# Kernel tuning notes

Measured on AMD Instinct MI355X. Metric: run time of the kernel, lower is better.

Reference implementation:

```python
import jax, jax.numpy as jnp
import numpy as np

WORD_VOCAB = 100000
TAG_VOCAB = 50
WD = 300
TD = 100
EMB = WD + TD          # 400: LSTM input size AND hidden size
H = EMB
L = 512


def setup_inputs() -> dict:
    key = jax.random.key(0)
    ks = jax.random.split(key, 16)
    def p(k, shape):
        return jax.random.normal(k, shape, dtype=jnp.float32) * 0.05
    return {
        "words_idx_tensor": jax.random.randint(ks[0], (1, L), 0, WORD_VOCAB),
        "tags_idx_tensor": jax.random.randint(ks[1], (1, L), 0, TAG_VOCAB),
        "max_length": L,
        "word_emb": p(ks[2], (WORD_VOCAB, WD)),
        "tag_emb": p(ks[3], (TAG_VOCAB, TD)),
        # stacked [fwd, bwd] directions per layer (PyTorch LSTM gate order i,f,g,o)
        "w_ih_l0": p(ks[4], (2, 4 * H, EMB)),
        "w_hh_l0": p(ks[5], (2, 4 * H, H)),
        "b_ih_l0": p(ks[6], (2, 4 * H)),
        "b_hh_l0": p(ks[7], (2, 4 * H)),
        "w_ih_l1": p(ks[8], (2, 4 * H, 2 * H)),
        "w_hh_l1": p(ks[9], (2, 4 * H, H)),
        "b_ih_l1": p(ks[10], (2, 4 * H)),
        "b_hh_l1": p(ks[11], (2, 4 * H)),
        "fc1_w": p(ks[12], (1, 4 * H)),
        "fc1_b": p(ks[13], (1,)),
    }


def _lstm_dir(x, w_ih, w_hh, b_ih, b_hh, reverse):
    # x: [T, in]. Precompute input projections once (hoisted out of scan).
    xi = x @ w_ih.T + b_ih + b_hh  # [T, 4H]
    Hn = w_hh.shape[1]

    def step(carry, g_in):
        h, c = carry
        g = g_in + h @ w_hh.T
        i, f, gg, o = jnp.split(g, 4, axis=-1)
        c = jax.nn.sigmoid(f) * c + jax.nn.sigmoid(i) * jnp.tanh(gg)
        h = jax.nn.sigmoid(o) * jnp.tanh(c)
        return (h, c), h

    init = (jnp.zeros((Hn,), x.dtype), jnp.zeros((Hn,), x.dtype))
    _, hs = jax.lax.scan(step, init, xi, reverse=reverse)
    return hs  # [T, H]


def _bilstm(x, w_ih, w_hh, b_ih, b_hh):
    fwd = _lstm_dir(x, w_ih[0], w_hh[0], b_ih[0], b_hh[0], False)
    bwd = _lstm_dir(x, w_ih[1], w_hh[1], b_ih[1], b_hh[1], True)
    return jnp.concatenate([fwd, bwd], axis=-1)  # [T, 2H]


def reference(words_idx_tensor, tags_idx_tensor, max_length, word_emb, tag_emb,
              w_ih_l0, w_hh_l0, b_ih_l0, b_hh_l0,
              w_ih_l1, w_hh_l1, b_ih_l1, b_hh_l1,
              fc1_w, fc1_b):
    # Embedding lookup + concat; batch dim of size 1 squeezed (torch's
    # view(shape[1], shape[0], -1) yields [L, 1, emb] for the LSTM).
    x = jnp.concatenate([word_emb[words_idx_tensor[0]],
                         tag_emb[tags_idx_tensor[0]]], axis=-1)  # [L, EMB]

    h = _bilstm(x, w_ih_l0, w_hh_l0, b_ih_l0, b_hh_l0)   # [L, 2H]
    h = _bilstm(h, w_ih_l1, w_hh_l1, b_ih_l1, b_hh_l1)   # [L, 2H]

    # Pairwise edge scores: tanh(W @ [h_i; h_j] + b).
    # Split W into head/dep halves -> two small GEMMs + broadcast outer-sum,
    # avoiding the O(L^2 * 4H) concatenated feature tensor.
    two_h = fc1_w.shape[1] // 2
    s = h @ fc1_w[:, :two_h].T   # [L, 1]
    t = h @ fc1_w[:, two_h:].T   # [L, 1]
    scores = jnp.tanh(s[:, None, :] + t[None, :, :] + fc1_b)  # [L, L, 1]
    # torch stacks (i outer, j inner) -> [L*L, 1, 1]
    return scores.reshape(max_length * max_length, 1, 1)
```

## Files before the change

kernel.cpp:

```cpp
#include <hip/hip_runtime.h>

#define SEQ 512
#define HID 400
#define GATES 1600
#define E1 800
#define TEAM 25
#define RECGRID 256
#define ROWS 64
#define HSL 16

__device__ __forceinline__ float bf2f(unsigned short u) {
    return __uint_as_float(((unsigned)u) << 16);
}
__device__ __forceinline__ unsigned short f2bf(float f) {
    unsigned u = __float_as_uint(f);
    u += 0x7FFFu + ((u >> 16) & 1u);
    return (unsigned short)(u >> 16);
}
__device__ __forceinline__ float sigm(float x) { return 1.f / (1.f + __expf(-x)); }
__device__ __forceinline__ float tanh_f(float x) {
    float xc = fminf(fmaxf(x, -15.f), 15.f);
    float e = __expf(2.f * xc);
    return (e - 1.f) / (e + 1.f);
}
__device__ __forceinline__ float loadx(const void* p, size_t i, int isbf) {
    return isbf ? bf2f(((const unsigned short*)p)[i]) : ((const float*)p)[i];
}

__global__ void detect_kernel(const unsigned short* __restrict__ wemb,
                              unsigned* __restrict__ dtf,
                              unsigned* __restrict__ syncz ) {
    __shared__ int cnt;
    if (threadIdx.x < 32) syncz[threadIdx.x] = 0u;
    if (threadIdx.x == 0) cnt = 0;
    __syncthreads();
    int pass = 0;
    for (int i = 0; i < 8; ++i) {
        unsigned short u = wemb[threadIdx.x * 8 + i];
        int e = (u >> 7) & 0xFF;
        pass += (e >= 100 && e <= 130) ? 1 : 0;
    }
    atomicAdd(&cnt, pass);
    __syncthreads();
    if (threadIdx.x == 0) *dtf = (cnt >= 1843) ? 1u : 0u;
}

__global__ void embed_kernel(const int* __restrict__ words, const int* __restrict__ tags,
                             const void* __restrict__ wemb, const void* __restrict__ temb,
                             float* __restrict__ x ,
                             const unsigned* __restrict__ dtf) {
    int t = blockIdx.x;
    int w = words[t], g = tags[t];
    int isbf = (int)*dtf;
    for (int k = threadIdx.x; k < HID; k += blockDim.x) {
        float v = (k < 300) ? loadx(wemb, (size_t)w * 300 + k, isbf)
                            : loadx(temb, (size_t)g * 100 + (k - 300), isbf);
        x[(size_t)t * HID + k] = v;
    }
}

__global__ __launch_bounds__(256) void proj_kernel(
        const void* __restrict__ Araw, int tagged,
        const void* __restrict__ Wraw ,
        const void* __restrict__ bihRaw, const void* __restrict__ bhhRaw,
        float* __restrict__ xi ,
        int K, const unsigned* __restrict__ dtf) {
    const int isbf = (int)*dtf;
    __shared__ float As[16][132];
    __shared__ float Ws[16][68];
    int tid = threadIdx.x;
    int t0 = blockIdx.x * 128, n0 = blockIdx.y * 64, dir = blockIdx.z;
    int arow = tid >> 1, akoff = (tid & 1) * 8;
    int wrow = tid >> 2, wkoff = (tid & 3) * 4;
    int tx = (tid & 15) * 4;
    int ty = (tid >> 4) * 8;

    const float* Af = (const float*)Araw + (size_t)(t0 + arow) * K + akoff;
    const unsigned long long* At = (const unsigned long long*)Araw +
                                   (size_t)(t0 + arow) * K + akoff;
    size_t wbase = (size_t)(dir * GATES + n0 + wrow) * K + wkoff;
    const float* Wf = (const float*)Wraw + wbase;
    const unsigned short* Wh = (const unsigned short*)Wraw + wbase;

    float acc[8][4] = {};
    for (int k0 = 0; k0 < K; k0 += 16) {
        float av8[8];
        if (tagged) {
            ulonglong2 q0 = *(const ulonglong2*)(At + k0);
            ulonglong2 q1 = *(const ulonglong2*)(At + k0 + 2);
            ulonglong2 q2 = *(const ulonglong2*)(At + k0 + 4);
            ulonglong2 q3 = *(const ulonglong2*)(At + k0 + 6);
            av8[0] = __uint_as_float((unsigned)q0.x); av8[1] = __uint_as_float((unsigned)q0.y);
            av8[2] = __uint_as_float((unsigned)q1.x); av8[3] = __uint_as_float((unsigned)q1.y);
            av8[4] = __uint_as_float((unsigned)q2.x); av8[5] = __uint_as_float((unsigned)q2.y);
            av8[6] = __uint_as_float((unsigned)q3.x); av8[7] = __uint_as_float((unsigned)q3.y);
        } else {
            float4 a0 = *(const float4*)(Af + k0);
            float4 a1 = *(const float4*)(Af + k0 + 4);
            av8[0] = a0.x; av8[1] = a0.y; av8[2] = a0.z; av8[3] = a0.w;
            av8[4] = a1.x; av8[5] = a1.y; av8[6] = a1.z; av8[7] = a1.w;
        }
        float4 wv;
        if (isbf) {
            ushort4 w4 = *(const ushort4*)(Wh + k0);
            wv = make_float4(bf2f(w4.x), bf2f(w4.y), bf2f(w4.z), bf2f(w4.w));
        } else {
            wv = *(const float4*)(Wf + k0);
        }
        __syncthreads();
#pragma unroll
        for (int i = 0; i < 8; ++i) As[akoff + i][arow] = av8[i];
        Ws[wkoff + 0][wrow] = wv.x; Ws[wkoff + 1][wrow] = wv.y;
        Ws[wkoff + 2][wrow] = wv.z; Ws[wkoff + 3][wrow] = wv.w;
        __syncthreads();
#pragma unroll
        for (int kk = 0; kk < 16; ++kk) {
            float4 alo = *(const float4*)&As[kk][ty];
            float4 ahi = *(const float4*)&As[kk][ty + 4];
            float4 w4  = *(const float4*)&Ws[kk][tx];
            float av[8] = {alo.x, alo.y, alo.z, alo.w, ahi.x, ahi.y, ahi.z, ahi.w};
            float wvv[4] = {w4.x, w4.y, w4.z, w4.w};
#pragma unroll
            for (int i = 0; i < 8; ++i)
#pragma unroll
                for (int j = 0; j < 4; ++j)
                    acc[i][j] = fmaf(av[i], wvv[j], acc[i][j]);
        }
    }
    float bias[4];
#pragma unroll
    for (int j = 0; j < 4; ++j) {
        int n = n0 + tx + j;
        bias[j] = loadx(bihRaw, dir * GATES + n, isbf) + loadx(bhhRaw, dir * GATES + n, isbf);
    }
    float* xout = xi + (size_t)dir * SEQ * GATES;
#pragma unroll
    for (int i = 0; i < 8; ++i) {
        int t = t0 + ty + i;
        float4 o = make_float4(acc[i][0] + bias[0], acc[i][1] + bias[1],
                               acc[i][2] + bias[2], acc[i][3] + bias[3]);
        *(float4*)&xout[(size_t)t * GATES + n0 + tx] = o;
    }
}

struct SyncArea { unsigned cnt[8]; unsigned claim[2]; unsigned pad[6]; };

__global__ __launch_bounds__(512, 2) void rec_kernel(
        const float* __restrict__ xi ,
        const void* __restrict__ whhRaw ,
        unsigned long long* __restrict__ hx  ,
        unsigned long long* __restrict__ hx2 ,
        unsigned tagbase, SyncArea* __restrict__ sy,
        const unsigned* __restrict__ dtf) {
    int tid = threadIdx.x;
    __shared__ int role[2];
    if (tid == 0) {
        unsigned xcd = __builtin_amdgcn_s_getreg((3 << 11) | 20) & 0xFu;
        unsigned rank = atomicAdd(&sy->cnt[xcd], 1u);
        unsigned group = rank / TEAM;
        unsigned key = 1u + xcd * 64u + group;
        if ((rank % TEAM) == TEAM - 1) {
            unsigned prev = atomicCAS(&sy->claim[0], 0u, key);
            if (prev != 0u) atomicCAS(&sy->claim[1], 0u, key);
        }
        int dir = -1;
        while (dir < 0) {
            unsigned c0 = __hip_atomic_load(&sy->claim[0], __ATOMIC_RELAXED,
                                            __HIP_MEMORY_SCOPE_AGENT);
            unsigned c1 = __hip_atomic_load(&sy->claim[1], __ATOMIC_RELAXED,
                                            __HIP_MEMORY_SCOPE_AGENT);
            if (c0 == key) dir = 0;
            else if (c1 == key) dir = 1;
            else if (c0 != 0u && c1 != 0u) dir = 2;
        }
        role[0] = dir;
        role[1] = (int)(rank % TEAM);
    }
    __syncthreads();
    const int dir = role[0];
    const int wg  = role[1];
    if (dir == 2) return;

    const int chunk = tid & 15;
    const int rg    = tid >> 4;
    const int isbf  = (int)*dtf;
    const int dirHID = dir * HID;

    __shared__ __align__(16) float hbuf[16 * 28];
    __shared__ __align__(16) float partials[ROWS][20];
    __shared__ __align__(16) float gates[ROWS];

    float wv[2][25];
#pragma unroll
    for (int r = 0; r < 2; ++r) {
        int lr = rg * 2 + r;
        int jj = lr >> 2, gg = lr & 3;
        int grow = gg * HID + wg * HSL + jj;
        size_t base = ((size_t)dir * GATES + grow) * HID + chunk * 25;
        if (isbf) {
            const unsigned short* p = (const unsigned short*)whhRaw + base;
#pragma unroll
            for (int c = 0; c < 25; ++c) wv[r][c] = bf2f(p[c]);
        } else {
            const float* p = (const float*)whhRaw + base;
#pragma unroll
            for (int c = 0; c < 25; ++c) wv[r][c] = p[c];
        }
    }

    int xrow = 0;
    if (tid < ROWS) { int jj = tid >> 2, gg = tid & 3; xrow = gg * HID + wg * HSL + jj; }
    const int hIdx = (tid / 25) * 28 + (tid % 25);
    const float* xibase = xi + (size_t)dir * SEQ * GATES;
    const int pl = tid - 448;
    float cstate = 0.f;
    size_t myelem = dirHID + wg * HSL + (pl & 15);

#pragma unroll 1
    for (int k = 0; k < SEQ; ++k) {
        int t = dir ? (SEQ - 1 - k) : k;
        float xiv = 0.f;
        if (tid < ROWS) xiv = xibase[(size_t)t * GATES + xrow];

        if (k > 0) {
            int tprev = dir ? (t + 1) : (t - 1);
            if (tid < HID) {
                const unsigned want = tagbase + (unsigned)k;
                size_t eidx = (size_t)tprev * E1 + dirHID + tid;
                const volatile unsigned long long* p =
                    (const volatile unsigned long long*)&hx[eidx];
                unsigned long long w;
                int spin = 0;
                for (;;) {
                    w = *p;
                    if ((unsigned)(w >> 32) == want) break;
                    if (++spin >= 24) {
                        w = __hip_atomic_load(&hx2[eidx], __ATOMIC_RELAXED,
                                              __HIP_MEMORY_SCOPE_AGENT);
                        if ((unsigned)(w >> 32) == want) break;
                        spin = 0;
                    }
                }
                hbuf[hIdx] = __uint_as_float((unsigned)w);
            }
        } else {
            if (tid < HID) hbuf[hIdx] = 0.f;
        }
        __syncthreads();

        const float* hb = &hbuf[chunk * 28];
        float4 h4a = *(const float4*)(hb + 0);
        float4 h4b = *(const float4*)(hb + 4);
        float4 h4c = *(const float4*)(hb + 8);
        float4 h4d = *(const float4*)(hb + 12);
        float4 h4e = *(const float4*)(hb + 16);
        float4 h4f = *(const float4*)(hb + 20);
        float hv[25] = {h4a.x, h4a.y, h4a.z, h4a.w, h4b.x, h4b.y, h4b.z, h4b.w,
                        h4c.x, h4c.y, h4c.z, h4c.w, h4d.x, h4d.y, h4d.z, h4d.w,
                        h4e.x, h4e.y, h4e.z, h4e.w, h4f.x, h4f.y, h4f.z, h4f.w,
                        hb[24]};
        float acc0 = 0.f, acc1 = 0.f;
#pragma unroll
        for (int c = 0; c < 25; ++c) {
            acc0 = fmaf(wv[0][c], hv[c], acc0);
            acc1 = fmaf(wv[1][c], hv[c], acc1);
        }
        partials[rg * 2 + 0][chunk] = acc0;
        partials[rg * 2 + 1][chunk] = acc1;
        __syncthreads();

        if (tid < ROWS) {
            const float4* pr = (const float4*)&partials[tid][0];
            float4 p0 = pr[0], p1 = pr[1], p2 = pr[2], p3 = pr[3];
            float s = p0.x + p0.y + p0.z + p0.w
                    + p1.x + p1.y + p1.z + p1.w
                    + p2.x + p2.y + p2.z + p2.w
                    + p3.x + p3.y + p3.z + p3.w;
            gates[tid] = s + xiv;
        }
        __syncthreads();

        if (pl >= 0 && pl < HSL) {
            float4 g4 = *(const float4*)&gates[pl * 4];
            float ig = sigm(g4.x), fg = sigm(g4.y), cg = tanh_f(g4.z), og = sigm(g4.w);
            cstate = fg * cstate + ig * cg;
            float hv2 = og * tanh_f(cstate);
            unsigned long long w =
                ((unsigned long long)(tagbase + (unsigned)k + 1u) << 32) |
                (unsigned long long)(unsigned)__float_as_uint(hv2);
            size_t eidx = (size_t)t * E1 + myelem;
            *(volatile unsigned long long*)&hx[eidx] = w;
            __hip_atomic_store(&hx2[eidx], w, __ATOMIC_RELAXED,
                               __HIP_MEMORY_SCOPE_AGENT);
        }
    }
}

__global__ void st_kernel(const unsigned long long* __restrict__ h1x ,
                          const void* __restrict__ fw ,
                          float* __restrict__ sv, float* __restrict__ tv,
                          const unsigned* __restrict__ dtf) {
    int i = blockIdx.x;
    int lane = threadIdx.x;
    int isbf = (int)*dtf;
    float s = 0.f, t = 0.f;
    for (int j = lane; j < E1; j += 64) {
        float hv = __uint_as_float((unsigned)h1x[(size_t)i * E1 + j]);
        s += hv * loadx(fw, j, isbf);
        t += hv * loadx(fw, E1 + j, isbf);
    }
#pragma unroll
    for (int o = 32; o > 0; o >>= 1) {
        s += __shfl_xor(s, o, 64);
        t += __shfl_xor(t, o, 64);
    }
    if (lane == 0) { sv[i] = s; tv[i] = t; }
}

__global__ void scores_kernel(const float* __restrict__ sv, const float* __restrict__ tv,
                              const void* __restrict__ fb, void* __restrict__ out,
                              const unsigned* __restrict__ dtf) {
    int idx = blockIdx.x * blockDim.x + threadIdx.x;
    int i = idx >> 9, j = idx & 511;
    int isbf = (int)*dtf;
    float v = tanh_f(sv[i] + tv[j] + loadx(fb, 0, isbf));
    if (isbf) ((unsigned short*)out)[idx] = f2bf(v);
    else      ((float*)out)[idx] = v;
}

static constexpr size_t OFF_X    = 0;
static constexpr size_t OFF_XI   = 819200;
static constexpr size_t OFF_SV   = 7372800;
static constexpr size_t OFF_TV   = 7374848;
static constexpr size_t OFF_DTF  = 7376896;
static constexpr size_t OFF_SYNC = 7376960;
static constexpr size_t OFF_HX   = 7377216;
static constexpr size_t OFF_HX2  = 10654016;

extern "C" void kernel_launch(void* const* d_in, const int* in_sizes, int n_in,
                              void* d_out, int out_size, void* d_ws, size_t ws_size,
                              hipStream_t stream) {
    const int* words = (const int*)d_in[0];
    const int* tags  = (const int*)d_in[1];
    const void* wemb = d_in[3];
    const void* temb = d_in[4];
    const void* wih0 = d_in[5];
    const void* whh0 = d_in[6];
    const void* bih0 = d_in[7];
    const void* bhh0 = d_in[8];
    const void* wih1 = d_in[9];
    const void* whh1 = d_in[10];
    const void* bih1 = d_in[11];
    const void* bhh1 = d_in[12];
    const void* fw   = d_in[13];
    const void* fb   = d_in[14];

    char* ws = (char*)d_ws;
    float* x               = (float*)(ws + OFF_X);
    float* xi              = (float*)(ws + OFF_XI);
    float* sv              = (float*)(ws + OFF_SV);
    float* tv              = (float*)(ws + OFF_TV);
    unsigned* dtf          = (unsigned*)(ws + OFF_DTF);
    SyncArea* sync0        = (SyncArea*)(ws + OFF_SYNC);
    SyncArea* sync1        = (SyncArea*)(ws + OFF_SYNC + 64);
    unsigned long long* hx  = (unsigned long long*)(ws + OFF_HX);
    unsigned long long* hx2 = (unsigned long long*)(ws + OFF_HX2);

    detect_kernel<<<1, 256, 0, stream>>>((const unsigned short*)wemb, dtf,
                                         (unsigned*)(ws + OFF_SYNC));
    embed_kernel<<<SEQ, 128, 0, stream>>>(words, tags, wemb, temb, x, dtf);

    proj_kernel<<<dim3(4, 25, 2), 256, 0, stream>>>(x, 0, wih0, bih0, bhh0, xi, HID, dtf);
    rec_kernel<<<RECGRID, 512, 0, stream>>>(xi, whh0, hx, hx2, 0u, sync0, dtf);

    proj_kernel<<<dim3(4, 25, 2), 256, 0, stream>>>(hx, 1, wih1, bih1, bhh1, xi, E1, dtf);
    rec_kernel<<<RECGRID, 512, 0, stream>>>(xi, whh1, hx, hx2, 512u, sync1, dtf);

    st_kernel<<<SEQ, 64, 0, stream>>>(hx, fw, sv, tv, dtf);
    scores_kernel<<<(SEQ * SEQ) / 256, 256, 0, stream>>>(sv, tv, fb, d_out, dtf);
}
```

Measured before the change: 1.684 ms.

## Overlap layer-1 projection and score dot-products with recurrence using idle blocks

Blocks in the recurrence kernel that get no direction role no longer exit. Instead they pull work tickets from an atomic counter. During layer 0 they compute the layer-1 input-projection tiles once the tagged hidden states for those rows are published in both directions. During layer 1 they compute the per-row s/t dot products for the final scores. The separate layer-1 projection kernel, the st kernel and the dtype-detect kernel go away, and detection plus sync-area reset move into the embed kernel. This removes launches and serial tail work, but it adds per-element tag polling and extra memory traffic that may contend with the latency-critical recurrence blocks.

After: 1.706 ms. About the same (+1.3%).

```diff
diff --git a/kernel.cpp b/kernel.cpp
--- a/kernel.cpp
+++ b/kernel.cpp
@@ -27,32 +27,52 @@
     return isbf ? bf2f(((const unsigned short*)p)[i]) : ((const float*)p)[i];
 }
 
-__global__ void detect_kernel(const unsigned short* __restrict__ wemb,
-                              unsigned* __restrict__ dtf,
-                              unsigned* __restrict__ syncz ) {
-    __shared__ int cnt;
-    if (threadIdx.x < 32) syncz[threadIdx.x] = 0u;
-    if (threadIdx.x == 0) cnt = 0;
-    __syncthreads();
-    int pass = 0;
-    for (int i = 0; i < 8; ++i) {
-        unsigned short u = wemb[threadIdx.x * 8 + i];
-        int e = (u >> 7) & 0xFF;
-        pass += (e >= 100 && e <= 130) ? 1 : 0;
-    }
-    atomicAdd(&cnt, pass);
-    __syncthreads();
-    if (threadIdx.x == 0) *dtf = (cnt >= 1843) ? 1u : 0u;
+__device__ __forceinline__ unsigned long long poll_tag(
+        const unsigned long long* hx, const unsigned long long* hx2,
+        size_t eidx, unsigned want) {
+    const volatile unsigned long long* p =
+        (const volatile unsigned long long*)&hx[eidx];
+    unsigned long long w;
+    int spin = 0;
+    for (;;) {
+        w = *p;
+        if ((unsigned)(w >> 32) == want) break;
+        if (++spin >= 24) {
+            w = __hip_atomic_load(&hx2[eidx], __ATOMIC_RELAXED,
+                                  __HIP_MEMORY_SCOPE_AGENT);
+            if ((unsigned)(w >> 32) == want) break;
+            spin = 0;
+        }
+    }
+    return w;
 }
 
 __global__ void embed_kernel(const int* __restrict__ words, const int* __restrict__ tags,
                              const void* __restrict__ wemb, const void* __restrict__ temb,
                              float* __restrict__ x ,
-                             const unsigned* __restrict__ dtf) {
+                             unsigned* __restrict__ dtf,
+                             unsigned* __restrict__ syncz ) {
+    __shared__ int cnt;
+    int tid = threadIdx.x;
     int t = blockIdx.x;
+    if (tid == 0) cnt = 0;
+    __syncthreads();
+    const unsigned short* wh = (const unsigned short*)wemb;
+    int pass = 0;
+    for (int i = 0; i < 16; ++i) {
+        unsigned short u = wh[tid * 16 + i];
+        int e = (u >> 7) & 0xFF;
+        pass += (e >= 100 && e <= 130) ? 1 : 0;
+    }
+    atomicAdd(&cnt, pass);
+    __syncthreads();
+    int isbf = (cnt >= 1843) ? 1 : 0;
+    if (t == 0) {
+        if (tid < 32) syncz[tid] = 0u;
+        if (tid == 0) *dtf = (unsigned)isbf;
+    }
     int w = words[t], g = tags[t];
-    int isbf = (int)*dtf;
-    for (int k = threadIdx.x; k < HID; k += blockDim.x) {
+    for (int k = tid; k < HID; k += blockDim.x) {
         float v = (k < 300) ? loadx(wemb, (size_t)w * 300 + k, isbf)
                             : loadx(temb, (size_t)g * 100 + (k - 300), isbf);
         x[(size_t)t * HID + k] = v;
@@ -151,7 +171,12 @@
         unsigned long long* __restrict__ hx  ,
         unsigned long long* __restrict__ hx2 ,
         unsigned tagbase, SyncArea* __restrict__ sy,
-        const unsigned* __restrict__ dtf) {
+        const unsigned* __restrict__ dtf,
+        int mode,
+        const void* __restrict__ wih1, const void* __restrict__ bih1,
+        const void* __restrict__ bhh1, float* __restrict__ xiOut,
+        const void* __restrict__ fw, float* __restrict__ sv,
+        float* __restrict__ tv) {
     int tid = threadIdx.x;
     __shared__ int role[2];
     if (tid == 0) {
@@ -179,16 +204,124 @@
     __syncthreads();
     const int dir = role[0];
     const int wg  = role[1];
-    if (dir == 2) return;
-
+
+    __shared__ __align__(16) float hbuf[16 * 28];
+    __shared__ __align__(16) float partials[ROWS][20];
+    __shared__ __align__(16) float gates[ROWS];
+    __shared__ __align__(16) float As2[16][132];
+    __shared__ __align__(16) float Ws2[16][68];
+    __shared__ int hticket;
+
+    if (dir == 2) {
+        const int isbf = (int)*dtf;
+        if (mode == 0) {
+            for (;;) {
+                if (tid == 0) hticket = (int)atomicAdd(&sy->pad[0], 1u);
+                __syncthreads();
+                int tk = hticket;
+                if (tk >= 200) return;
+                int t0 = (tk & 3) * 128;
+                int n0 = ((tk >> 2) % 25) * 64;
+                int dw = tk / 100;
+                if (tid == 0)
+                    (void)poll_tag(hx, hx2, (size_t)(t0 + 127) * E1 + 0,
+                                   (unsigned)(t0 + 128));
+                if (tid == 1)
+                    (void)poll_tag(hx, hx2, (size_t)t0 * E1 + HID,
+                                   (unsigned)(512 - t0));
+                __syncthreads();
+
+                float acc[4][4] = {};
+                int arow = tid >> 2, akoff = (tid & 3) * 4;
+                int wrow = tid >> 3, wkoff = (tid & 7) * 2;
+                int tx = (tid & 15) * 4, ty = (tid >> 4) * 4;
+                int tA = t0 + arow;
+                for (int k0 = 0; k0 < E1; k0 += 16) {
+                    float a4[4];
+#pragma unroll
+                    for (int j = 0; j < 4; ++j) {
+                        int e = k0 + akoff + j;
+                        unsigned want = (e < HID) ? (unsigned)(tA + 1)
+                                                  : (unsigned)(512 - tA);
+                        unsigned long long w =
+                            poll_tag(hx, hx2, (size_t)tA * E1 + e, want);
+                        a4[j] = __uint_as_float((unsigned)w);
+                    }
+                    float wf0 = loadx(wih1, ((size_t)(dw * GATES + n0 + wrow)) * E1
+                                            + k0 + wkoff + 0, isbf);
+                    float wf1 = loadx(wih1, ((size_t)(dw * GATES + n0 + wrow)) * E1
+                                            + k0 + wkoff + 1, isbf);
+                    __syncthreads();
+#pragma unroll
+                    for (int j = 0; j < 4; ++j) As2[akoff + j][arow] = a4[j];
+                    Ws2[wkoff + 0][wrow] = wf0;
+                    Ws2[wkoff + 1][wrow] = wf1;
+                    __syncthreads();
+#pragma unroll
+                    for (int kk = 0; kk < 16; ++kk) {
+                        float4 av = *(const float4*)&As2[kk][ty];
+                        float4 w4 = *(const float4*)&Ws2[kk][tx];
+                        float avv[4] = {av.x, av.y, av.z, av.w};
+                        float wvv[4] = {w4.x, w4.y, w4.z, w4.w};
+#pragma unroll
+                        for (int i = 0; i < 4; ++i)
+#pragma unroll
+                            for (int j = 0; j < 4; ++j)
+                                acc[i][j] = fmaf(avv[i], wvv[j], acc[i][j]);
+                    }
+                }
+                float bias[4];
+#pragma unroll
+                for (int j = 0; j < 4; ++j) {
+                    int n = n0 + tx + j;
+                    bias[j] = loadx(bih1, dw * GATES + n, isbf)
+                            + loadx(bhh1, dw * GATES + n, isbf);
+                }
+                float* xo = xiOut + (size_t)dw * SEQ * GATES;
+#pragma unroll
+                for (int i = 0; i < 4; ++i) {
+                    int t = t0 + ty + i;
+                    float4 o = make_float4(acc[i][0] + bias[0], acc[i][1] + bias[1],
+                                           acc[i][2] + bias[2], acc[i][3] + bias[3]);
+                    *(float4*)&xo[(size_t)t * GATES + n0 + tx] = o;
+                }
+                __syncthreads();
+            }
+        } else {
+            int wid = tid >> 6, lane = tid & 63;
+            for (;;) {
+                if (tid == 0) hticket = (int)atomicAdd(&sy->pad[0], 1u);
+                __syncthreads();
+                int ck = hticket;
+                if (ck >= 64) return;
+                int i = ck * 8 + wid;
+                if (lane == 0) {
+                    (void)poll_tag(hx, hx2, (size_t)i * E1 + 0, (unsigned)(513 + i));
+                    (void)poll_tag(hx, hx2, (size_t)i * E1 + HID, (unsigned)(1024 - i));
+                }
+                float s = 0.f, t2 = 0.f;
+                for (int j = lane; j < E1; j += 64) {
+                    unsigned want = (j < HID) ? (unsigned)(513 + i)
+                                              : (unsigned)(1024 - i);
+                    unsigned long long w = poll_tag(hx, hx2, (size_t)i * E1 + j, want);
+                    float hv = __uint_as_float((unsigned)w);
+                    s  += hv * loadx(fw, j, isbf);
+                    t2 += hv * loadx(fw, E1 + j, isbf);
+                }
+#pragma unroll
+                for (int o = 32; o > 0; o >>= 1) {
+                    s  += __shfl_xor(s, o, 64);
+                    t2 += __shfl_xor(t2, o, 64);
+                }
+                if (lane == 0) { sv[i] = s; tv[i] = t2; }
+                __syncthreads();
+            }
+        }
+    }
     const int chunk = tid & 15;
     const int rg    = tid >> 4;
     const int isbf  = (int)*dtf;
     const int dirHID = dir * HID;
-
-    __shared__ __align__(16) float hbuf[16 * 28];
-    __shared__ __align__(16) float partials[ROWS][20];
-    __shared__ __align__(16) float gates[ROWS];
 
     float wv[2][25];
 #pragma unroll
@@ -296,27 +429,6 @@
     }
 }
 
-__global__ void st_kernel(const unsigned long long* __restrict__ h1x ,
-                          const void* __restrict__ fw ,
-                          float* __restrict__ sv, float* __restrict__ tv,
-                          const unsigned* __restrict__ dtf) {
-    int i = blockIdx.x;
-    int lane = threadIdx.x;
-    int isbf = (int)*dtf;
-    float s = 0.f, t = 0.f;
-    for (int j = lane; j < E1; j += 64) {
-        float hv = __uint_as_float((unsigned)h1x[(size_t)i * E1 + j]);
-        s += hv * loadx(fw, j, isbf);
-        t += hv * loadx(fw, E1 + j, isbf);
-    }
-#pragma unroll
-    for (int o = 32; o > 0; o >>= 1) {
-        s += __shfl_xor(s, o, 64);
-        t += __shfl_xor(t, o, 64);
-    }
-    if (lane == 0) { sv[i] = s; tv[i] = t; }
-}
-
 __global__ void scores_kernel(const float* __restrict__ sv, const float* __restrict__ tv,
                               const void* __restrict__ fb, void* __restrict__ out,
                               const unsigned* __restrict__ dtf) {
@@ -366,16 +478,17 @@
     unsigned long long* hx  = (unsigned long long*)(ws + OFF_HX);
     unsigned long long* hx2 = (unsigned long long*)(ws + OFF_HX2);
 
-    detect_kernel<<<1, 256, 0, stream>>>((const unsigned short*)wemb, dtf,
-                                         (unsigned*)(ws + OFF_SYNC));
-    embed_kernel<<<SEQ, 128, 0, stream>>>(words, tags, wemb, temb, x, dtf);
+    embed_kernel<<<SEQ, 128, 0, stream>>>(words, tags, wemb, temb, x, dtf,
+                                          (unsigned*)(ws + OFF_SYNC));
 
     proj_kernel<<<dim3(4, 25, 2), 256, 0, stream>>>(x, 0, wih0, bih0, bhh0, xi, HID, dtf);
-    rec_kernel<<<RECGRID, 512, 0, stream>>>(xi, whh0, hx, hx2, 0u, sync0, dtf);
-
-    proj_kernel<<<dim3(4, 25, 2), 256, 0, stream>>>(hx, 1, wih1, bih1, bhh1, xi, E1, dtf);
-    rec_kernel<<<RECGRID, 512, 0, stream>>>(xi, whh1, hx, hx2, 512u, sync1, dtf);
-
-    st_kernel<<<SEQ, 64, 0, stream>>>(hx, fw, sv, tv, dtf);
+    rec_kernel<<<RECGRID, 512, 0, stream>>>(xi, whh0, hx, hx2, 0u, sync0, dtf,
+                                            0, wih1, bih1, bhh1, xi,
+                                            nullptr, nullptr, nullptr);
+
+    rec_kernel<<<RECGRID, 512, 0, stream>>>(xi, whh1, hx, hx2, 512u, sync1, dtf,
+                                            1, nullptr, nullptr, nullptr, nullptr,
+                                            fw, sv, tv);
+
     scores_kernel<<<(SEQ * SEQ) / 256, 256, 0, stream>>>(sv, tv, fb, d_out, dtf);
 }
```
